# Performance work log

Hardware: AMD Instinct MI355X
Metric: run time of the kernel (lower is better)

## Reference

```python
import jax, jax.numpy as jnp
import numpy as np

N = 50000          # num nodes
E = 800000         # num edges (before self-loops)
F_IN = 128
H = 4              # heads
C1 = 16            # hidden channels per head
C2 = 8             # out channels per head
NEG_SLOPE = 0.2
EPS = 1e-16


def setup_inputs() -> dict:
    key = jax.random.key(0)
    ks = jax.random.split(key, 10)
    x = jax.random.normal(ks[0], (N, F_IN), dtype=jnp.float32)
    edge_index = jax.random.randint(ks[1], (2, E), 0, N, dtype=jnp.int64)
    s1 = 1.0 / np.sqrt(F_IN)
    s2 = 1.0 / np.sqrt(H * C1)
    return {
        "x": x,
        "edge_index": edge_index,
        "W1": jax.random.normal(ks[2], (F_IN, H * C1), dtype=jnp.float32) * s1,
        "a_src1": jax.random.normal(ks[3], (H, C1), dtype=jnp.float32) * s2,
        "a_dst1": jax.random.normal(ks[4], (H, C1), dtype=jnp.float32) * s2,
        "b1": jnp.zeros((H * C1,), dtype=jnp.float32),
        "W2": jax.random.normal(ks[5], (H * C1, H * C2), dtype=jnp.float32) * s2,
        "a_src2": jax.random.normal(ks[6], (H, C2), dtype=jnp.float32) * 0.2,
        "a_dst2": jax.random.normal(ks[7], (H, C2), dtype=jnp.float32) * 0.2,
        "b2": jnp.zeros((H * C2,), dtype=jnp.float32),
    }


def _gat_conv(x, src, dst, W, a_src, a_dst, b, heads, ch):
    # linear transform -> per-head features [N, H, C]
    h = (x @ W).reshape(-1, heads, ch)
    # per-node attention logits [N, H]
    al_src = jnp.sum(h * a_src[None], axis=-1)
    al_dst = jnp.sum(h * a_dst[None], axis=-1)
    # edge-wise logits + leaky relu [E, H]
    e = al_src[src] + al_dst[dst]
    e = jnp.where(e >= 0, e, NEG_SLOPE * e)
    # segment softmax over destination neighborhoods
    m = jax.ops.segment_max(e, dst, num_segments=N)
    e = jnp.exp(e - m[dst])
    s = jax.ops.segment_sum(e, dst, num_segments=N)
    alpha = e / (s[dst] + EPS)                      # [E, H]
    # weighted gather-scatter aggregate [N, H, C]
    msg = h[src] * alpha[..., None]
    out = jax.ops.segment_sum(msg, dst, num_segments=N)
    # concat heads + bias
    return out.reshape(-1, heads * ch) + b


def reference(x, edge_index, W1, a_src1, a_dst1, b1, W2, a_src2, a_dst2, b2):
    # PyG GATConv adds self-loops by default
    loop = jnp.arange(N, dtype=edge_index.dtype)
    src = jnp.concatenate([edge_index[0], loop])
    dst = jnp.concatenate([edge_index[1], loop])
    h = _gat_conv(x, src, dst, W1, a_src1, a_dst1, b1, H, C1)
    h = jax.nn.relu(h)
    h = _gat_conv(h, src, dst, W2, a_src2, a_dst2, b2, H, C2)
    return jax.nn.log_softmax(h, axis=1)
```

## Files before the change

### kernel.cpp

```cpp
#include <hip/hip_runtime.h>
#include <hip/hip_bf16.h>
#include <math.h>

#define NN 50000
#define NE 800000
#define ET (NE + NN)
#define DCAP 128
#define SG 196
#define ECH 8192
#define NCH 104
#define NPASS 8
#define NRANGE 6250

#define NCV 3321
#define NG1 1563
#define SPLITB (3 * NG1)
#define TOTB (NCV + NG1)

__device__ __forceinline__ float bf2f(unsigned short u) {
    return __uint_as_float(((unsigned)u) << 16);
}
__device__ __forceinline__ unsigned short f2bf(float f) {
    unsigned u = __float_as_uint(f);
    return (unsigned short)((u + 0x7fff + ((u >> 16) & 1)) >> 16);
}
__device__ __forceinline__ float lrelu(float e) {
    return e >= 0.f ? e : 0.2f * e;
}

__global__ __launch_bounds__(256) void k_front(const void* __restrict__ xraw,
                                               const void* __restrict__ ei,
                                               const void* p2, const void* p3, const void* p4, const void* p5,
                                               const void* p6, const void* p7, const void* p8, const void* p9,
                                               int2* __restrict__ pairs, int* __restrict__ deg,
                                               float* __restrict__ wsm,
                                               unsigned short* __restrict__ h1b,
                                               float* __restrict__ als, float* __restrict__ ald) {
    __shared__ unsigned int Wp[64 * 65];
    __shared__ float xt[32 * 132];
    __shared__ int wred[8];
    int t = threadIdx.x;
    int b = blockIdx.x;

    const unsigned long long* e64 = (const unsigned long long*)ei;
    const unsigned int* x32 = (const unsigned int*)xraw;
    int ci = 0, cf = 0;
    #pragma unroll
    for (int q = 0; q < 4; q++) {
        if (e64[4 * t + q] >= (unsigned long long)NN) ci = 1;
        unsigned ex = (x32[4 * t + q] >> 7) & 0xFFu;
        cf += (ex >= 96 && ex <= 140) ? 1 : 0;
    }
    #pragma unroll
    for (int off = 32; off; off >>= 1) { ci |= __shfl_xor(ci, off); cf += __shfl_xor(cf, off); }
    if ((t & 63) == 0) { wred[t >> 6] = ci; wred[4 + (t >> 6)] = cf; }
    __syncthreads();
    int iflag = (wred[0] | wred[1] | wred[2] | wred[3]) ? 0 : 1;
    int fl = ((wred[4] + wred[5] + wred[6] + wred[7]) > 700) ? 1 : 0;

    int role, id;
    if (b < SPLITB) {
        int g = b / 3, r = b % 3;
        if (r == 2) { role = 1; id = g; }
        else        { role = 0; id = 2 * g + r; }
    } else {
        role = 0; id = b - NG1;
    }

    if (role == 0) {
        int e = id * 256 + t;
        if (e < 10528) {
            const void* p; int off;
            if (e < 8192)       { p = p2; off = e; }
            else if (e < 8256)  { p = p3; off = e - 8192; }
            else if (e < 8320)  { p = p4; off = e - 8256; }
            else if (e < 8384)  { p = p5; off = e - 8320; }
            else if (e < 10432) { p = p6; off = e - 8384; }
            else if (e < 10464) { p = p7; off = e - 10432; }
            else if (e < 10496) { p = p8; off = e - 10464; }
            else                { p = p9; off = e - 10496; }
            wsm[e] = fl ? bf2f(((const unsigned short*)p)[off]) : ((const float*)p)[off];
        }
        if (e >= ET) return;
        int s, d;
        if (e >= NE) { s = d = e - NE; }
        else if (iflag) {
            s = (int)((const long long*)ei)[e];
            d = (int)((const long long*)ei)[NE + e];
        } else {
            s = ((const int*)ei)[e];
            d = ((const int*)ei)[NE + e];
        }
        pairs[e] = make_int2(s, d);
        atomicAdd(&deg[d], 1);
        return;
    }

    const void* w1raw = p2; const void* as1raw = p3; const void* ad1raw = p4;
    int rb = id * 32;
    for (int i = t; i < 64 * 64; i += 256) {
        int k2 = i >> 6, c = i & 63;
        unsigned lo, hi;
        if (fl) {
            lo = ((const unsigned short*)w1raw)[(2 * k2) * 64 + c];
            hi = ((const unsigned short*)w1raw)[(2 * k2 + 1) * 64 + c];
        } else {
            lo = f2bf(((const float*)w1raw)[(2 * k2) * 64 + c]);
            hi = f2bf(((const float*)w1raw)[(2 * k2 + 1) * 64 + c]);
        }
        Wp[c * 65 + k2] = lo | (hi << 16);
    }
    if (fl) {
        const unsigned short* xb = (const unsigned short*)xraw;
        for (int i = t; i < 32 * 16; i += 256) {
            int r = i >> 4, k8 = i & 15;
            float f[8];
            if (rb + r < NN) {
                uint4 v = ((const uint4*)xb)[(size_t)(rb + r) * 16 + k8];
                f[0] = bf2f((unsigned short)(v.x & 0xffff)); f[1] = bf2f((unsigned short)(v.x >> 16));
                f[2] = bf2f((unsigned short)(v.y & 0xffff)); f[3] = bf2f((unsigned short)(v.y >> 16));
                f[4] = bf2f((unsigned short)(v.z & 0xffff)); f[5] = bf2f((unsigned short)(v.z >> 16));
                f[6] = bf2f((unsigned short)(v.w & 0xffff)); f[7] = bf2f((unsigned short)(v.w >> 16));
            } else {
                #pragma unroll
                for (int q = 0; q < 8; q++) f[q] = 0.f;
            }
            int o = r * 132 + k8 * 8;
            *(float4*)&xt[o]     = make_float4(f[0], f[1], f[2], f[3]);
            *(float4*)&xt[o + 4] = make_float4(f[4], f[5], f[6], f[7]);
        }
    } else {
        const float* xf = (const float*)xraw;
        for (int i = t; i < 32 * 32; i += 256) {
            int r = i >> 5, kq = i & 31;
            float4 v = make_float4(0.f, 0.f, 0.f, 0.f);
            if (rb + r < NN) v = ((const float4*)xf)[(size_t)(rb + r) * 32 + kq];
            *(float4*)&xt[r * 132 + kq * 4] = v;
        }
    }
    __syncthreads();
    int c = t & 63;
    int rg = t >> 6;
    float acc[8];
    #pragma unroll
    for (int j = 0; j < 8; j++) acc[j] = 0.f;
    for (int k2 = 0; k2 < 64; k2 += 2) {
        unsigned q0 = Wp[c * 65 + k2];
        unsigned q1 = Wp[c * 65 + k2 + 1];
        float w0 = __uint_as_float(q0 << 16);
        float w1 = __uint_as_float(q0 & 0xffff0000u);
        float w2 = __uint_as_float(q1 << 16);
        float w3 = __uint_as_float(q1 & 0xffff0000u);
        int kk = k2 * 2;
        #pragma unroll
        for (int j = 0; j < 8; j++) {
            float4 xv = *(const float4*)&xt[(rg * 8 + j) * 132 + kk];
            acc[j] = fmaf(xv.x, w0, fmaf(xv.y, w1, fmaf(xv.z, w2, fmaf(xv.w, w3, acc[j]))));
        }
    }
    float asf = fl ? bf2f(((const unsigned short*)as1raw)[c]) : ((const float*)as1raw)[c];
    float adf = fl ? bf2f(((const unsigned short*)ad1raw)[c]) : ((const float*)ad1raw)[c];
    #pragma unroll
    for (int j = 0; j < 8; j++) {
        int r = rb + rg * 8 + j;
        bool ok = r < NN;
        if (ok) h1b[(size_t)r * 64 + c] = f2bf(acc[j]);
        float v = acc[j] * asf, w = acc[j] * adf;
        #pragma unroll
        for (int off = 1; off < 16; off <<= 1) {
            v += __shfl_xor(v, off);
            w += __shfl_xor(w, off);
        }
        if (ok && (c & 15) == 0) {
            als[r * 4 + (c >> 4)] = v;
            ald[r * 4 + (c >> 4)] = w;
        }
    }
}

__device__ __forceinline__ int block_excl_scan(int v, int* lds, int t) {
    int lane = t & 63, wid = t >> 6;
    int inc = v;
    #pragma unroll
    for (int d = 1; d < 64; d <<= 1) {
        int u = __shfl_up(inc, d);
        if (lane >= d) inc += u;
    }
    if (lane == 63) lds[wid] = inc;
    __syncthreads();
    if (t == 0) {
        int a = lds[0], b = lds[1], c = lds[2];
        lds[4] = 0; lds[5] = a; lds[6] = a + b; lds[7] = a + b + c;
    }
    __syncthreads();
    return lds[4 + wid] + inc - v;
}

__global__ __launch_bounds__(256) void k_scan(const int* __restrict__ deg, int* __restrict__ bsum,
                                              int* __restrict__ ctr,
                                              int* __restrict__ rs, int* __restrict__ cur) {
    __shared__ int lds[8];
    __shared__ int sOff, sTot;
    int t = threadIdx.x, b = blockIdx.x;
    int i = b * 256 + t;
    int v = (i < NN) ? deg[i] : 0;
    int e_loc = block_excl_scan(v, lds, t);
    if (t == 255) {
        bsum[b] = e_loc + v;
        __threadfence();
        atomicAdd(ctr, 1);
    }
    if (t == 0) {
        while (__hip_atomic_load(ctr, __ATOMIC_ACQUIRE, __HIP_MEMORY_SCOPE_AGENT) < SG) {
            __builtin_amdgcn_s_sleep(1);
        }
    }
    __syncthreads();
    __threadfence();
    int bv = (t < SG) ? bsum[t] : 0;
    int be = block_excl_scan(bv, lds, t);
    if (t == b) sOff = be;
    if (t == SG - 1) sTot = be + bv;
    __syncthreads();
    int e = sOff + e_loc;
    if (i < NN) {
        rs[i] = e; cur[i] = e;
        if (i == NN - 1) rs[NN] = sTot;
    }
}

__global__ __launch_bounds__(256) void k_scatter8(const int2* __restrict__ pairs,
                                                  int* __restrict__ cur, int* __restrict__ csr) {
    int b = blockIdx.x;
    int pass = b & (NPASS - 1);
    int chunk = b >> 3;
    int lo = pass * NRANGE, hi = lo + NRANGE;
    int base = chunk * ECH;
    for (int i = threadIdx.x; i < ECH; i += 256) {
        int e = base + i;
        if (e < ET) {
            int2 pr = pairs[e];
            if (pr.y >= lo && pr.y < hi) {
                int pos = atomicAdd(&cur[pr.y], 1);
                csr[pos] = pr.x;
            }
        }
    }
}

__global__ __launch_bounds__(256) void k_gemm2(const float* __restrict__ in,
                                               const float* __restrict__ Wf,
                                               const float* __restrict__ asf_p,
                                               const float* __restrict__ adf_p,
                                               unsigned short* __restrict__ h2b,
                                               float* __restrict__ als, float* __restrict__ ald) {
    __shared__ float Wt[32 * 65];
    __shared__ float xt[64 * 68];
    int tid = threadIdx.x;
    int rb = blockIdx.x * 64;
    for (int i = tid; i < 64 * 32; i += 256) {
        int k = i >> 5, c = i & 31;
        Wt[c * 65 + k] = Wf[i];
    }
    for (int i = tid; i < 64 * 16; i += 256) {
        int r = i >> 4, kq = i & 15;
        float4 v = make_float4(0.f, 0.f, 0.f, 0.f);
        if (rb + r < NN) v = ((const float4*)in)[(size_t)(rb + r) * 16 + kq];
        *(float4*)&xt[r * 68 + kq * 4] = v;
    }
    __syncthreads();
    int c = tid & 31, rg = tid >> 5;
    float acc[8];
    #pragma unroll
    for (int j = 0; j < 8; j++) acc[j] = 0.f;
    #pragma unroll 2
    for (int k = 0; k < 64; k += 4) {
        float4 w;
        w.x = Wt[c * 65 + k];     w.y = Wt[c * 65 + k + 1];
        w.z = Wt[c * 65 + k + 2]; w.w = Wt[c * 65 + k + 3];
        #pragma unroll
        for (int j = 0; j < 8; j++) {
            float4 xv = *(const float4*)&xt[(rg * 8 + j) * 68 + k];
            acc[j] = fmaf(xv.x, w.x, fmaf(xv.y, w.y, fmaf(xv.z, w.z, fmaf(xv.w, w.w, acc[j]))));
        }
    }
    float asf = asf_p[c], adf = adf_p[c];
    #pragma unroll
    for (int j = 0; j < 8; j++) {
        int r = rb + rg * 8 + j;
        bool ok = r < NN;
        if (ok) h2b[(size_t)r * 32 + c] = f2bf(acc[j]);
        float v = acc[j] * asf, w = acc[j] * adf;
        #pragma unroll
        for (int off = 1; off < 8; off <<= 1) {
            v += __shfl_xor(v, off);
            w += __shfl_xor(w, off);
        }
        if (ok && (c & 7) == 0) {
            als[r * 4 + (c >> 3)] = v;
            ald[r * 4 + (c >> 3)] = w;
        }
    }
}

__global__ __launch_bounds__(256) void k_agg1(const int* __restrict__ rs, const int* __restrict__ csr,
                                              const float* __restrict__ als, const float* __restrict__ aldv,
                                              const unsigned short* __restrict__ h1b,
                                              const float* __restrict__ b1,
                                              float* __restrict__ out1) {
    __shared__ float pv[4][DCAP * 4];
    __shared__ int  sidx[4][DCAP];
    int w = threadIdx.x >> 6, lane = threadIdx.x & 63;
    int n = blockIdx.x * 4 + w;
    if (n >= NN) return;
    int base = rs[n];
    int deg = rs[n + 1] - base;
    float4 ald = *(const float4*)(aldv + 4 * n);

    if (deg <= DCAP) {
        int sA = 0;
        bool v0 = lane < deg, v1 = lane + 64 < deg;
        if (v0) {
            sA = csr[base + lane];
            sidx[w][lane] = sA;
            float4 a = *(const float4*)(als + 4 * sA);
            float4 p;
            p.x = __expf(lrelu(a.x + ald.x)); p.y = __expf(lrelu(a.y + ald.y));
            p.z = __expf(lrelu(a.z + ald.z)); p.w = __expf(lrelu(a.w + ald.w));
            *(float4*)&pv[w][lane * 4] = p;
        }
        if (v1) {
            int sB = csr[base + lane + 64];
            sidx[w][lane + 64] = sB;
            float4 a = *(const float4*)(als + 4 * sB);
            float4 p;
            p.x = __expf(lrelu(a.x + ald.x)); p.y = __expf(lrelu(a.y + ald.y));
            p.z = __expf(lrelu(a.z + ald.z)); p.w = __expf(lrelu(a.w + ald.w));
            *(float4*)&pv[w][(lane + 64) * 4] = p;
        }
        int degp = (deg + 3) & ~3;
        int s0v = __shfl(sA, 0);
        if (lane >= deg && lane < degp) {
            sidx[w][lane] = s0v;
            *(float4*)&pv[w][lane * 4] = make_float4(0.f, 0.f, 0.f, 0.f);
        }
        int i1 = lane + 64;
        if (i1 >= deg && i1 < degp) {
            sidx[w][i1] = s0v;
            *(float4*)&pv[w][i1 * 4] = make_float4(0.f, 0.f, 0.f, 0.f);
        }
        int g = lane >> 4, j = lane & 15, hh = j >> 2;
        float4 a4 = make_float4(0.f, 0.f, 0.f, 0.f);
        float ps = 0.f;
        for (int e = 0; e < degp; e += 4) {
            int s = sidx[w][e + g];
            float ph = pv[w][(e + g) * 4 + hh];
            uint2 rv = *(const uint2*)&h1b[(size_t)s * 64 + j * 4];
            ps += ph;
            a4.x = fmaf(ph, bf2f((unsigned short)(rv.x & 0xffff)), a4.x);
            a4.y = fmaf(ph, bf2f((unsigned short)(rv.x >> 16)),    a4.y);
            a4.z = fmaf(ph, bf2f((unsigned short)(rv.y & 0xffff)), a4.z);
            a4.w = fmaf(ph, bf2f((unsigned short)(rv.y >> 16)),    a4.w);
        }
        #pragma unroll
        for (int off = 16; off <= 32; off <<= 1) {
            a4.x += __shfl_xor(a4.x, off);
            a4.y += __shfl_xor(a4.y, off);
            a4.z += __shfl_xor(a4.z, off);
            a4.w += __shfl_xor(a4.w, off);
            ps   += __shfl_xor(ps,   off);
        }
        if (g == 0) {
            float rh = 1.f / (ps + 1e-16f);
            float4 bb = *(const float4*)&b1[j * 4];
            float4 o;
            o.x = fmaxf(a4.x * rh + bb.x, 0.f);
            o.y = fmaxf(a4.y * rh + bb.y, 0.f);
            o.z = fmaxf(a4.z * rh + bb.z, 0.f);
            o.w = fmaxf(a4.w * rh + bb.w, 0.f);
            *(float4*)&out1[(size_t)n * 64 + j * 4] = o;
        }
    } else {
        int h = lane >> 4;
        float s0 = 0.f, s1 = 0.f, s2 = 0.f, s3 = 0.f;
        for (int i = lane; i < deg; i += 64) {
            int s = csr[base + i];
            float4 a = *(const float4*)(als + 4 * s);
            s0 += __expf(lrelu(a.x + ald.x));
            s1 += __expf(lrelu(a.y + ald.y));
            s2 += __expf(lrelu(a.z + ald.z));
            s3 += __expf(lrelu(a.w + ald.w));
        }
        #pragma unroll
        for (int off = 32; off; off >>= 1) {
            s0 += __shfl_xor(s0, off);
            s1 += __shfl_xor(s1, off);
            s2 += __shfl_xor(s2, off);
            s3 += __shfl_xor(s3, off);
        }
        float sh = (h == 0) ? s0 : (h == 1) ? s1 : (h == 2) ? s2 : s3;
        float ah = (h == 0) ? ald.x : (h == 1) ? ald.y : (h == 2) ? ald.z : ald.w;
        float rh = 1.f / (sh + 1e-16f);
        float acc = 0.f;
        for (int e = 0; e < deg; ++e) {
            int s = csr[base + e];
            float av = als[4 * s + h];
            float ph = __expf(lrelu(av + ah));
            acc = fmaf(ph, bf2f(h1b[(size_t)s * 64 + lane]), acc);
        }
        out1[(size_t)n * 64 + lane] = fmaxf(acc * rh + b1[lane], 0.f);
    }
}

__global__ __launch_bounds__(256) void k_agg2(const int* __restrict__ rs, const int* __restrict__ csr,
                                              const float* __restrict__ als, const float* __restrict__ aldv,
                                              const unsigned short* __restrict__ h2b,
                                              const float* __restrict__ b2,
                                              float* __restrict__ out) {
    __shared__ float pv[4][DCAP * 4];
    __shared__ int  sidx[4][DCAP];
    int w = threadIdx.x >> 6, lane = threadIdx.x & 63;
    int n = blockIdx.x * 4 + w;
    if (n >= NN) return;
    int base = rs[n];
    int deg = rs[n + 1] - base;
    float4 ald = *(const float4*)(aldv + 4 * n);

    if (deg <= DCAP) {
        int sA = 0;
        bool v0 = lane < deg, v1 = lane + 64 < deg;
        if (v0) {
            sA = csr[base + lane];
            sidx[w][lane] = sA;
            float4 a = *(const float4*)(als + 4 * sA);
            float4 p;
            p.x = __expf(lrelu(a.x + ald.x)); p.y = __expf(lrelu(a.y + ald.y));
            p.z = __expf(lrelu(a.z + ald.z)); p.w = __expf(lrelu(a.w + ald.w));
            *(float4*)&pv[w][lane * 4] = p;
        }
        if (v1) {
            int sB = csr[base + lane + 64];
            sidx[w][lane + 64] = sB;
            float4 a = *(const float4*)(als + 4 * sB);
            float4 p;
            p.x = __expf(lrelu(a.x + ald.x)); p.y = __expf(lrelu(a.y + ald.y));
            p.z = __expf(lrelu(a.z + ald.z)); p.w = __expf(lrelu(a.w + ald.w));
            *(float4*)&pv[w][(lane + 64) * 4] = p;
        }
        int degp = (deg + 7) & ~7;
        int s0v = __shfl(sA, 0);
        if (lane >= deg && lane < degp) {
            sidx[w][lane] = s0v;
            *(float4*)&pv[w][lane * 4] = make_float4(0.f, 0.f, 0.f, 0.f);
        }
        int i1 = lane + 64;
        if (i1 >= deg && i1 < degp) {
            sidx[w][i1] = s0v;
            *(float4*)&pv[w][i1 * 4] = make_float4(0.f, 0.f, 0.f, 0.f);
        }
        int g = lane >> 3, j = lane & 7, hh = j >> 1;
        float4 a4 = make_float4(0.f, 0.f, 0.f, 0.f);
        float ps = 0.f;
        for (int e = 0; e < degp; e += 8) {
            int s = sidx[w][e + g];
            float ph = pv[w][(e + g) * 4 + hh];
            uint2 rv = *(const uint2*)&h2b[(size_t)s * 32 + j * 4];
            ps += ph;
            a4.x = fmaf(ph, bf2f((unsigned short)(rv.x & 0xffff)), a4.x);
            a4.y = fmaf(ph, bf2f((unsigned short)(rv.x >> 16)),    a4.y);
            a4.z = fmaf(ph, bf2f((unsigned short)(rv.y & 0xffff)), a4.z);
            a4.w = fmaf(ph, bf2f((unsigned short)(rv.y >> 16)),    a4.w);
        }
        #pragma unroll
        for (int off = 8; off <= 32; off <<= 1) {
            a4.x += __shfl_xor(a4.x, off);
            a4.y += __shfl_xor(a4.y, off);
            a4.z += __shfl_xor(a4.z, off);
            a4.w += __shfl_xor(a4.w, off);
            ps   += __shfl_xor(ps,   off);
        }
        float rh = 1.f / (ps + 1e-16f);
        float4 bb = *(const float4*)&b2[j * 4];
        float4 row;
        row.x = a4.x * rh + bb.x; row.y = a4.y * rh + bb.y;
        row.z = a4.z * rh + bb.z; row.w = a4.w * rh + bb.w;
        float mx = fmaxf(fmaxf(row.x, row.y), fmaxf(row.z, row.w));
        #pragma unroll
        for (int off = 1; off < 8; off <<= 1) mx = fmaxf(mx, __shfl_xor(mx, off));
        float sm = __expf(row.x - mx) + __expf(row.y - mx)
                 + __expf(row.z - mx) + __expf(row.w - mx);
        #pragma unroll
        for (int off = 1; off < 8; off <<= 1) sm += __shfl_xor(sm, off);
        float lse = mx + logf(sm);
        if (g == 0) {
            float4 o;
            o.x = row.x - lse; o.y = row.y - lse;
            o.z = row.z - lse; o.w = row.w - lse;
            *(float4*)&out[(size_t)n * 32 + j * 4] = o;
        }
    } else {
        float s0 = 0.f, s1 = 0.f, s2 = 0.f, s3 = 0.f;
        for (int i = lane; i < deg; i += 64) {
            int s = csr[base + i];
            float4 a = *(const float4*)(als + 4 * s);
            s0 += __expf(lrelu(a.x + ald.x));
            s1 += __expf(lrelu(a.y + ald.y));
            s2 += __expf(lrelu(a.z + ald.z));
            s3 += __expf(lrelu(a.w + ald.w));
        }
        #pragma unroll
        for (int off = 32; off; off >>= 1) {
            s0 += __shfl_xor(s0, off);
            s1 += __shfl_xor(s1, off);
            s2 += __shfl_xor(s2, off);
            s3 += __shfl_xor(s3, off);
        }
        int L = lane & 31;
        int h2i = L >> 3;
        float sh2 = (h2i == 0) ? s0 : (h2i == 1) ? s1 : (h2i == 2) ? s2 : s3;
        float ah2 = (h2i == 0) ? ald.x : (h2i == 1) ? ald.y : (h2i == 2) ? ald.z : ald.w;
        float rh2 = 1.f / (sh2 + 1e-16f);
        if (lane < 32) {
            float acc = 0.f;
            for (int e = 0; e < deg; ++e) {
                int s = csr[base + e];
                float av = als[4 * s + h2i];
                float ph = __expf(lrelu(av + ah2));
                acc = fmaf(ph, bf2f(h2b[(size_t)s * 32 + L]), acc);
            }
            float row = acc * rh2 + b2[L];
            float mx = row;
            #pragma unroll
            for (int off = 16; off; off >>= 1) mx = fmaxf(mx, __shfl_xor(mx, off, 32));
            float pe = __expf(row - mx);
            float sm = pe;
            #pragma unroll
            for (int off = 16; off; off >>= 1) sm += __shfl_xor(sm, off, 32);
            out[(size_t)n * 32 + L] = row - mx - logf(sm);
        }
    }
}

extern "C" void kernel_launch(void* const* d_in, const int* in_sizes, int n_in,
                              void* d_out, int out_size, void* d_ws, size_t ws_size,
                              hipStream_t stream) {
    const void* x  = d_in[0];
    const void* ei = d_in[1];
    float* out = (float*)d_out;

    char* p = (char*)d_ws;
    auto take = [&](size_t b) -> char* {
        char* r = p; p += (b + 255) & ~(size_t)255; return r;
    };
    int*   degc  = (int*)take(sizeof(int) * (NN + 8));
    int*   deg   = degc;
    int*   ctr   = degc + NN;
    int*   rs    = (int*)take(sizeof(int) * (NN + 1));
    int*   cur   = (int*)take(sizeof(int) * NN);
    int*   bsum  = (int*)take(sizeof(int) * 256);
    int2*  pairs = (int2*)take(sizeof(int2) * ET);
    int*   csr   = (int*)take(sizeof(int) * ET);
    float* wsm   = (float*)take(sizeof(float) * 10528);
    unsigned short* h1b = (unsigned short*)take(sizeof(unsigned short) * (size_t)NN * 64);
    float* als1  = (float*)take(sizeof(float) * NN * 4);
    float* ald1  = (float*)take(sizeof(float) * NN * 4);
    float* out1  = (float*)take(sizeof(float) * (size_t)NN * 64);
    unsigned short* h2b = (unsigned short*)take(sizeof(unsigned short) * (size_t)NN * 32);
    float* als2  = (float*)take(sizeof(float) * NN * 4);
    float* ald2  = (float*)take(sizeof(float) * NN * 4);

    float* Wf2  = wsm + 8384;
    float* as2f = wsm + 10432;
    float* ad2f = wsm + 10464;
    float* b1f  = wsm + 8320;
    float* b2f  = wsm + 10496;

    hipMemsetAsync(degc, 0, sizeof(int) * (NN + 8), stream);
    k_front<<<TOTB, 256, 0, stream>>>(x, ei, d_in[2], d_in[3], d_in[4], d_in[5],
                                      d_in[6], d_in[7], d_in[8], d_in[9],
                                      pairs, deg, wsm, h1b, als1, ald1);
    k_scan<<<SG, 256, 0, stream>>>(deg, bsum, ctr, rs, cur);
    k_scatter8<<<NPASS * NCH, 256, 0, stream>>>(pairs, cur, csr);

    k_agg1<<<(NN + 3) / 4, 256, 0, stream>>>(rs, csr, als1, ald1, h1b, b1f, out1);

    k_gemm2<<<(NN + 63) / 64, 256, 0, stream>>>(out1, Wf2, as2f, ad2f, h2b, als2, ald2);
    k_agg2<<<(NN + 3) / 4, 256, 0, stream>>>(rs, csr, als2, ald2, h2b, b2f, out);
}
```

Baseline: 276.2 us.

## Fuse CSR build into one persistent kernel with grid barriers, split out GEMM1

Edge pair extraction, degree counting, the prefix scan and the CSR scatter now run in a single 832-block kernel that uses atomic-counter grid barriers between phases, in place of three separate launches. The first-layer GEMM moves into its own kernel launched first. Before, the GEMM was interleaved with the edge work inside one launch. The aim is to cut launch gaps and tail effects. The grid barriers are safe only if all 832 blocks are co-resident, and the fused kernel loses the overlap with GEMM1 it had before.

After: 629.0 us. 128% more time.

```diff
diff --git a/kernel.cpp b/kernel.cpp
--- a/kernel.cpp
+++ b/kernel.cpp
@@ -11,11 +11,8 @@
 #define NCH 104
 #define NPASS 8
 #define NRANGE 6250
-
-#define NCV 3321
+#define CSRB (NPASS * NCH)
 #define NG1 1563
-#define SPLITB (3 * NG1)
-#define TOTB (NCV + NG1)
 
 __device__ __forceinline__ float bf2f(unsigned short u) {
     return __uint_as_float(((unsigned)u) << 16);
@@ -28,19 +25,50 @@
     return e >= 0.f ? e : 0.2f * e;
 }
 
-__global__ __launch_bounds__(256) void k_front(const void* __restrict__ xraw,
-                                               const void* __restrict__ ei,
-                                               const void* p2, const void* p3, const void* p4, const void* p5,
-                                               const void* p6, const void* p7, const void* p8, const void* p9,
-                                               int2* __restrict__ pairs, int* __restrict__ deg,
-                                               float* __restrict__ wsm,
-                                               unsigned short* __restrict__ h1b,
-                                               float* __restrict__ als, float* __restrict__ ald) {
-    __shared__ unsigned int Wp[64 * 65];
-    __shared__ float xt[32 * 132];
+__device__ __forceinline__ int block_excl_scan(int v, int* lds, int t) {
+    int lane = t & 63, wid = t >> 6;
+    int inc = v;
+    #pragma unroll
+    for (int d = 1; d < 64; d <<= 1) {
+        int u = __shfl_up(inc, d);
+        if (lane >= d) inc += u;
+    }
+    if (lane == 63) lds[wid] = inc;
+    __syncthreads();
+    if (t == 0) {
+        int a = lds[0], b = lds[1], c = lds[2];
+        lds[4] = 0; lds[5] = a; lds[6] = a + b; lds[7] = a + b + c;
+    }
+    __syncthreads();
+    return lds[4 + wid] + inc - v;
+}
+
+__device__ __forceinline__ void gbar(int* ctr, int target) {
+    __syncthreads();
+    if (threadIdx.x == 0) {
+        __threadfence();
+        atomicAdd(ctr, 1);
+        while (__hip_atomic_load(ctr, __ATOMIC_ACQUIRE, __HIP_MEMORY_SCOPE_AGENT) < target) {
+            __builtin_amdgcn_s_sleep(1);
+        }
+    }
+    __syncthreads();
+    __threadfence();
+}
+
+__global__ __launch_bounds__(256) void k_csr(const void* __restrict__ xraw,
+                                             const void* __restrict__ ei,
+                                             const void* p2, const void* p3, const void* p4, const void* p5,
+                                             const void* p6, const void* p7, const void* p8, const void* p9,
+                                             int2* __restrict__ pairs, int* __restrict__ deg,
+                                             float* __restrict__ wsm, int* __restrict__ bsum,
+                                             int* __restrict__ ctrA, int* __restrict__ ctrS, int* __restrict__ ctrB,
+                                             int* __restrict__ rs, int* __restrict__ cur,
+                                             int* __restrict__ csr) {
+    __shared__ int lds[8];
     __shared__ int wred[8];
-    int t = threadIdx.x;
-    int b = blockIdx.x;
+    __shared__ int sOff, sTot;
+    int t = threadIdx.x, b = blockIdx.x;
 
     const unsigned long long* e64 = (const unsigned long long*)ei;
     const unsigned int* x32 = (const unsigned int*)xraw;
@@ -58,17 +86,7 @@
     int iflag = (wred[0] | wred[1] | wred[2] | wred[3]) ? 0 : 1;
     int fl = ((wred[4] + wred[5] + wred[6] + wred[7]) > 700) ? 1 : 0;
 
-    int role, id;
-    if (b < SPLITB) {
-        int g = b / 3, r = b % 3;
-        if (r == 2) { role = 1; id = g; }
-        else        { role = 0; id = 2 * g + r; }
-    } else {
-        role = 0; id = b - NG1;
-    }
-
-    if (role == 0) {
-        int e = id * 256 + t;
+    for (int e = b * 256 + t; e < ET; e += CSRB * 256) {
         if (e < 10528) {
             const void* p; int off;
             if (e < 8192)       { p = p2; off = e; }
@@ -81,7 +99,6 @@
             else                { p = p9; off = e - 10496; }
             wsm[e] = fl ? bf2f(((const unsigned short*)p)[off]) : ((const float*)p)[off];
         }
-        if (e >= ET) return;
         int s, d;
         if (e >= NE) { s = d = e - NE; }
         else if (iflag) {
@@ -93,12 +110,84 @@
         }
         pairs[e] = make_int2(s, d);
         atomicAdd(&deg[d], 1);
-        return;
-    }
-
-    const void* w1raw = p2; const void* as1raw = p3; const void* ad1raw = p4;
-    int rb = id * 32;
-    for (int i = t; i < 64 * 64; i += 256) {
+    }
+
+    gbar(ctrA, CSRB);
+
+    if (b < SG) {
+        int i = b * 256 + t;
+        int v = (i < NN) ? deg[i] : 0;
+        int e_loc = block_excl_scan(v, lds, t);
+        if (t == 255) {
+            bsum[b] = e_loc + v;
+            __threadfence();
+            atomicAdd(ctrS, 1);
+        }
+        if (t == 0) {
+            while (__hip_atomic_load(ctrS, __ATOMIC_ACQUIRE, __HIP_MEMORY_SCOPE_AGENT) < SG) {
+                __builtin_amdgcn_s_sleep(1);
+            }
+        }
+        __syncthreads();
+        __threadfence();
+        int bv = (t < SG) ? bsum[t] : 0;
+        int be = block_excl_scan(bv, lds, t);
+        if (t == b) sOff = be;
+        if (t == SG - 1) sTot = be + bv;
+        __syncthreads();
+        int e = sOff + e_loc;
+        if (i < NN) {
+            rs[i] = e; cur[i] = e;
+            if (i == NN - 1) rs[NN] = sTot;
+        }
+    }
+
+    gbar(ctrB, CSRB);
+
+    {
+        int pass = b & (NPASS - 1);
+        int chunk = b >> 3;
+        int lo = pass * NRANGE, hi = lo + NRANGE;
+        int base = chunk * ECH;
+        for (int i = t; i < ECH; i += 256) {
+            int e = base + i;
+            if (e < ET) {
+                int2 pr = pairs[e];
+                if (pr.y >= lo && pr.y < hi) {
+                    int pos = atomicAdd(&cur[pr.y], 1);
+                    csr[pos] = pr.x;
+                }
+            }
+        }
+    }
+}
+
+__global__ __launch_bounds__(256) void k_gemm1(const void* __restrict__ xraw,
+                                               const void* __restrict__ w1raw,
+                                               const void* __restrict__ as1raw,
+                                               const void* __restrict__ ad1raw,
+                                               unsigned short* __restrict__ h1b,
+                                               float* __restrict__ als, float* __restrict__ ald) {
+    __shared__ unsigned int Wp[64 * 65];
+    __shared__ float xt[32 * 132];
+    __shared__ int wred[4];
+    int tid = threadIdx.x;
+    int rb = blockIdx.x * 32;
+
+    const unsigned int* x32 = (const unsigned int*)xraw;
+    int cf = 0;
+    #pragma unroll
+    for (int q = 0; q < 4; q++) {
+        unsigned ex = (x32[4 * tid + q] >> 7) & 0xFFu;
+        cf += (ex >= 96 && ex <= 140) ? 1 : 0;
+    }
+    #pragma unroll
+    for (int off = 32; off; off >>= 1) cf += __shfl_xor(cf, off);
+    if ((tid & 63) == 0) wred[tid >> 6] = cf;
+    __syncthreads();
+    int fl = ((wred[0] + wred[1] + wred[2] + wred[3]) > 700) ? 1 : 0;
+
+    for (int i = tid; i < 64 * 64; i += 256) {
         int k2 = i >> 6, c = i & 63;
         unsigned lo, hi;
         if (fl) {
@@ -112,7 +201,7 @@
     }
     if (fl) {
         const unsigned short* xb = (const unsigned short*)xraw;
-        for (int i = t; i < 32 * 16; i += 256) {
+        for (int i = tid; i < 32 * 16; i += 256) {
             int r = i >> 4, k8 = i & 15;
             float f[8];
             if (rb + r < NN) {
@@ -131,7 +220,7 @@
         }
     } else {
         const float* xf = (const float*)xraw;
-        for (int i = t; i < 32 * 32; i += 256) {
+        for (int i = tid; i < 32 * 32; i += 256) {
             int r = i >> 5, kq = i & 31;
             float4 v = make_float4(0.f, 0.f, 0.f, 0.f);
             if (rb + r < NN) v = ((const float4*)xf)[(size_t)(rb + r) * 32 + kq];
@@ -139,8 +228,8 @@
         }
     }
     __syncthreads();
-    int c = t & 63;
-    int rg = t >> 6;
+    int c = tid & 63;
+    int rg = tid >> 6;
     float acc[8];
     #pragma unroll
     for (int j = 0; j < 8; j++) acc[j] = 0.f;
@@ -174,76 +263,6 @@
         if (ok && (c & 15) == 0) {
             als[r * 4 + (c >> 4)] = v;
             ald[r * 4 + (c >> 4)] = w;
-        }
-    }
-}
-
-__device__ __forceinline__ int block_excl_scan(int v, int* lds, int t) {
-    int lane = t & 63, wid = t >> 6;
-    int inc = v;
-    #pragma unroll
-    for (int d = 1; d < 64; d <<= 1) {
-        int u = __shfl_up(inc, d);
-        if (lane >= d) inc += u;
-    }
-    if (lane == 63) lds[wid] = inc;
-    __syncthreads();
-    if (t == 0) {
-        int a = lds[0], b = lds[1], c = lds[2];
-        lds[4] = 0; lds[5] = a; lds[6] = a + b; lds[7] = a + b + c;
-    }
-    __syncthreads();
-    return lds[4 + wid] + inc - v;
-}
-
-__global__ __launch_bounds__(256) void k_scan(const int* __restrict__ deg, int* __restrict__ bsum,
-                                              int* __restrict__ ctr,
-                                              int* __restrict__ rs, int* __restrict__ cur) {
-    __shared__ int lds[8];
-    __shared__ int sOff, sTot;
-    int t = threadIdx.x, b = blockIdx.x;
-    int i = b * 256 + t;
-    int v = (i < NN) ? deg[i] : 0;
-    int e_loc = block_excl_scan(v, lds, t);
-    if (t == 255) {
-        bsum[b] = e_loc + v;
-        __threadfence();
-        atomicAdd(ctr, 1);
-    }
-    if (t == 0) {
-        while (__hip_atomic_load(ctr, __ATOMIC_ACQUIRE, __HIP_MEMORY_SCOPE_AGENT) < SG) {
-            __builtin_amdgcn_s_sleep(1);
-        }
-    }
-    __syncthreads();
-    __threadfence();
-    int bv = (t < SG) ? bsum[t] : 0;
-    int be = block_excl_scan(bv, lds, t);
-    if (t == b) sOff = be;
-    if (t == SG - 1) sTot = be + bv;
-    __syncthreads();
-    int e = sOff + e_loc;
-    if (i < NN) {
-        rs[i] = e; cur[i] = e;
-        if (i == NN - 1) rs[NN] = sTot;
-    }
-}
-
-__global__ __launch_bounds__(256) void k_scatter8(const int2* __restrict__ pairs,
-                                                  int* __restrict__ cur, int* __restrict__ csr) {
-    int b = blockIdx.x;
-    int pass = b & (NPASS - 1);
-    int chunk = b >> 3;
-    int lo = pass * NRANGE, hi = lo + NRANGE;
-    int base = chunk * ECH;
-    for (int i = threadIdx.x; i < ECH; i += 256) {
-        int e = base + i;
-        if (e < ET) {
-            int2 pr = pairs[e];
-            if (pr.y >= lo && pr.y < hi) {
-                int pos = atomicAdd(&cur[pr.y], 1);
-                csr[pos] = pr.x;
-            }
         }
     }
 }
@@ -554,7 +573,9 @@
     };
     int*   degc  = (int*)take(sizeof(int) * (NN + 8));
     int*   deg   = degc;
-    int*   ctr   = degc + NN;
+    int*   ctrA  = degc + NN;
+    int*   ctrS  = degc + NN + 1;
+    int*   ctrB  = degc + NN + 2;
     int*   rs    = (int*)take(sizeof(int) * (NN + 1));
     int*   cur   = (int*)take(sizeof(int) * NN);
     int*   bsum  = (int*)take(sizeof(int) * 256);
@@ -576,11 +597,10 @@
     float* b2f  = wsm + 10496;
 
     hipMemsetAsync(degc, 0, sizeof(int) * (NN + 8), stream);
-    k_front<<<TOTB, 256, 0, stream>>>(x, ei, d_in[2], d_in[3], d_in[4], d_in[5],
-                                      d_in[6], d_in[7], d_in[8], d_in[9],
-                                      pairs, deg, wsm, h1b, als1, ald1);
-    k_scan<<<SG, 256, 0, stream>>>(deg, bsum, ctr, rs, cur);
-    k_scatter8<<<NPASS * NCH, 256, 0, stream>>>(pairs, cur, csr);
+    k_gemm1<<<NG1, 256, 0, stream>>>(x, d_in[2], d_in[3], d_in[4], h1b, als1, ald1);
+    k_csr<<<CSRB, 256, 0, stream>>>(x, ei, d_in[2], d_in[3], d_in[4], d_in[5],
+                                    d_in[6], d_in[7], d_in[8], d_in[9],
+                                    pairs, deg, wsm, bsum, ctrA, ctrS, ctrB, rs, cur, csr);
 
     k_agg1<<<(NN + 3) / 4, 256, 0, stream>>>(rs, csr, als1, ald1, h1b, b1f, out1);
 
```

## Replace CSR scan/scatter with fixed-capacity per-node adjacency plus overflow list

Applied to the files above, without the earlier changes.

Drops the degree prefix scan and the multi-pass scatter kernels. Each edge now claims a slot in a fixed 48-entry row per destination node via atomicAdd and is written straight there, or into a global overflow list once the row is full. The aggregation kernels read these rows directly and, for high-degree nodes, linearly scan the overflow list. This removes two launches and the pairs buffer in exchange for a larger, sparser adjacency array, a capacity limit of 8192 overflow edges, and a costly linear overflow scan for the few high-degree nodes.

After: 225.0 us. -18.6%, faster.

```diff
diff --git a/kernel.cpp b/kernel.cpp
--- a/kernel.cpp
+++ b/kernel.cpp
@@ -5,17 +5,9 @@
 #define NN 50000
 #define NE 800000
 #define ET (NE + NN)
-#define DCAP 128
-#define SG 196
-#define ECH 8192
-#define NCH 104
-#define NPASS 8
-#define NRANGE 6250
-
-#define NCV 3321
+#define DCAP 48
+#define MAXOVF 8192
 #define NG1 1563
-#define SPLITB (3 * NG1)
-#define TOTB (NCV + NG1)
 
 __device__ __forceinline__ float bf2f(unsigned short u) {
     return __uint_as_float(((unsigned)u) << 16);
@@ -28,77 +20,39 @@
     return e >= 0.f ? e : 0.2f * e;
 }
 
-__global__ __launch_bounds__(256) void k_front(const void* __restrict__ xraw,
-                                               const void* __restrict__ ei,
-                                               const void* p2, const void* p3, const void* p4, const void* p5,
-                                               const void* p6, const void* p7, const void* p8, const void* p9,
-                                               int2* __restrict__ pairs, int* __restrict__ deg,
-                                               float* __restrict__ wsm,
-                                               unsigned short* __restrict__ h1b,
-                                               float* __restrict__ als, float* __restrict__ ald) {
+__global__ __launch_bounds__(256) void k_gemm1cv(const void* __restrict__ xraw,
+                                                 const void* __restrict__ ei,
+                                                 const void* p2, const void* p3, const void* p4, const void* p5,
+                                                 const void* p6, const void* p7, const void* p8, const void* p9,
+                                                 unsigned short* __restrict__ h1b,
+                                                 float* __restrict__ als, float* __restrict__ ald,
+                                                 int* __restrict__ csrF, int* __restrict__ deg,
+                                                 int2* __restrict__ ovf, int* __restrict__ ovfcnt,
+                                                 float* __restrict__ wsm) {
     __shared__ unsigned int Wp[64 * 65];
     __shared__ float xt[32 * 132];
     __shared__ int wred[8];
-    int t = threadIdx.x;
-    int b = blockIdx.x;
-
-    const unsigned long long* e64 = (const unsigned long long*)ei;
+    int tid = threadIdx.x;
+    int rb = blockIdx.x * 32;
+
+    const unsigned long long* e64u = (const unsigned long long*)ei;
     const unsigned int* x32 = (const unsigned int*)xraw;
     int ci = 0, cf = 0;
     #pragma unroll
     for (int q = 0; q < 4; q++) {
-        if (e64[4 * t + q] >= (unsigned long long)NN) ci = 1;
-        unsigned ex = (x32[4 * t + q] >> 7) & 0xFFu;
+        if (e64u[4 * tid + q] >= (unsigned long long)NN) ci = 1;
+        unsigned ex = (x32[4 * tid + q] >> 7) & 0xFFu;
         cf += (ex >= 96 && ex <= 140) ? 1 : 0;
     }
     #pragma unroll
     for (int off = 32; off; off >>= 1) { ci |= __shfl_xor(ci, off); cf += __shfl_xor(cf, off); }
-    if ((t & 63) == 0) { wred[t >> 6] = ci; wred[4 + (t >> 6)] = cf; }
+    if ((tid & 63) == 0) { wred[tid >> 6] = ci; wred[4 + (tid >> 6)] = cf; }
     __syncthreads();
     int iflag = (wred[0] | wred[1] | wred[2] | wred[3]) ? 0 : 1;
     int fl = ((wred[4] + wred[5] + wred[6] + wred[7]) > 700) ? 1 : 0;
 
-    int role, id;
-    if (b < SPLITB) {
-        int g = b / 3, r = b % 3;
-        if (r == 2) { role = 1; id = g; }
-        else        { role = 0; id = 2 * g + r; }
-    } else {
-        role = 0; id = b - NG1;
-    }
-
-    if (role == 0) {
-        int e = id * 256 + t;
-        if (e < 10528) {
-            const void* p; int off;
-            if (e < 8192)       { p = p2; off = e; }
-            else if (e < 8256)  { p = p3; off = e - 8192; }
-            else if (e < 8320)  { p = p4; off = e - 8256; }
-            else if (e < 8384)  { p = p5; off = e - 8320; }
-            else if (e < 10432) { p = p6; off = e - 8384; }
-            else if (e < 10464) { p = p7; off = e - 10432; }
-            else if (e < 10496) { p = p8; off = e - 10464; }
-            else                { p = p9; off = e - 10496; }
-            wsm[e] = fl ? bf2f(((const unsigned short*)p)[off]) : ((const float*)p)[off];
-        }
-        if (e >= ET) return;
-        int s, d;
-        if (e >= NE) { s = d = e - NE; }
-        else if (iflag) {
-            s = (int)((const long long*)ei)[e];
-            d = (int)((const long long*)ei)[NE + e];
-        } else {
-            s = ((const int*)ei)[e];
-            d = ((const int*)ei)[NE + e];
-        }
-        pairs[e] = make_int2(s, d);
-        atomicAdd(&deg[d], 1);
-        return;
-    }
-
     const void* w1raw = p2; const void* as1raw = p3; const void* ad1raw = p4;
-    int rb = id * 32;
-    for (int i = t; i < 64 * 64; i += 256) {
+    for (int i = tid; i < 64 * 64; i += 256) {
         int k2 = i >> 6, c = i & 63;
         unsigned lo, hi;
         if (fl) {
@@ -112,7 +66,7 @@
     }
     if (fl) {
         const unsigned short* xb = (const unsigned short*)xraw;
-        for (int i = t; i < 32 * 16; i += 256) {
+        for (int i = tid; i < 32 * 16; i += 256) {
             int r = i >> 4, k8 = i & 15;
             float f[8];
             if (rb + r < NN) {
@@ -131,7 +85,7 @@
         }
     } else {
         const float* xf = (const float*)xraw;
-        for (int i = t; i < 32 * 32; i += 256) {
+        for (int i = tid; i < 32 * 32; i += 256) {
             int r = i >> 5, kq = i & 31;
             float4 v = make_float4(0.f, 0.f, 0.f, 0.f);
             if (rb + r < NN) v = ((const float4*)xf)[(size_t)(rb + r) * 32 + kq];
@@ -139,8 +93,8 @@
         }
     }
     __syncthreads();
-    int c = t & 63;
-    int rg = t >> 6;
+    int c = tid & 63;
+    int rg = tid >> 6;
     float acc[8];
     #pragma unroll
     for (int j = 0; j < 8; j++) acc[j] = 0.f;
@@ -176,75 +130,151 @@
             ald[r * 4 + (c >> 4)] = w;
         }
     }
-}
-
-__device__ __forceinline__ int block_excl_scan(int v, int* lds, int t) {
-    int lane = t & 63, wid = t >> 6;
-    int inc = v;
-    #pragma unroll
-    for (int d = 1; d < 64; d <<= 1) {
-        int u = __shfl_up(inc, d);
-        if (lane >= d) inc += u;
-    }
-    if (lane == 63) lds[wid] = inc;
-    __syncthreads();
-    if (t == 0) {
-        int a = lds[0], b = lds[1], c = lds[2];
-        lds[4] = 0; lds[5] = a; lds[6] = a + b; lds[7] = a + b + c;
-    }
-    __syncthreads();
-    return lds[4 + wid] + inc - v;
-}
-
-__global__ __launch_bounds__(256) void k_scan(const int* __restrict__ deg, int* __restrict__ bsum,
-                                              int* __restrict__ ctr,
-                                              int* __restrict__ rs, int* __restrict__ cur) {
-    __shared__ int lds[8];
-    __shared__ int sOff, sTot;
-    int t = threadIdx.x, b = blockIdx.x;
-    int i = b * 256 + t;
-    int v = (i < NN) ? deg[i] : 0;
-    int e_loc = block_excl_scan(v, lds, t);
-    if (t == 255) {
-        bsum[b] = e_loc + v;
-        __threadfence();
-        atomicAdd(ctr, 1);
-    }
-    if (t == 0) {
-        while (__hip_atomic_load(ctr, __ATOMIC_ACQUIRE, __HIP_MEMORY_SCOPE_AGENT) < SG) {
-            __builtin_amdgcn_s_sleep(1);
-        }
-    }
-    __syncthreads();
-    __threadfence();
-    int bv = (t < SG) ? bsum[t] : 0;
-    int be = block_excl_scan(bv, lds, t);
-    if (t == b) sOff = be;
-    if (t == SG - 1) sTot = be + bv;
-    __syncthreads();
-    int e = sOff + e_loc;
-    if (i < NN) {
-        rs[i] = e; cur[i] = e;
-        if (i == NN - 1) rs[NN] = sTot;
-    }
-}
-
-__global__ __launch_bounds__(256) void k_scatter8(const int2* __restrict__ pairs,
-                                                  int* __restrict__ cur, int* __restrict__ csr) {
-    int b = blockIdx.x;
-    int pass = b & (NPASS - 1);
-    int chunk = b >> 3;
-    int lo = pass * NRANGE, hi = lo + NRANGE;
-    int base = chunk * ECH;
-    for (int i = threadIdx.x; i < ECH; i += 256) {
-        int e = base + i;
-        if (e < ET) {
-            int2 pr = pairs[e];
-            if (pr.y >= lo && pr.y < hi) {
-                int pos = atomicAdd(&cur[pr.y], 1);
-                csr[pos] = pr.x;
+
+    const long long* e64s = (const long long*)ei;
+    for (int e = blockIdx.x * 256 + tid; e < ET; e += NG1 * 256) {
+        if (e < 10528) {
+            const void* p; int off;
+            if (e < 8192)       { p = p2; off = e; }
+            else if (e < 8256)  { p = p3; off = e - 8192; }
+            else if (e < 8320)  { p = p4; off = e - 8256; }
+            else if (e < 8384)  { p = p5; off = e - 8320; }
+            else if (e < 10432) { p = p6; off = e - 8384; }
+            else if (e < 10464) { p = p7; off = e - 10432; }
+            else if (e < 10496) { p = p8; off = e - 10464; }
+            else                { p = p9; off = e - 10496; }
+            wsm[e] = fl ? bf2f(((const unsigned short*)p)[off]) : ((const float*)p)[off];
+        }
+        int s, d;
+        if (e >= NE) { s = d = e - NE; }
+        else if (iflag) {
+            s = (int)e64s[e];
+            d = (int)e64s[NE + e];
+        } else {
+            s = ((const int*)ei)[e];
+            d = ((const int*)ei)[NE + e];
+        }
+        int slot = atomicAdd(&deg[d], 1);
+        if (slot < DCAP) csrF[(size_t)d * DCAP + slot] = s;
+        else {
+            int o = atomicAdd(ovfcnt, 1);
+            if (o < MAXOVF) ovf[o] = make_int2(s, d);
+        }
+    }
+}
+
+__global__ __launch_bounds__(256) void k_agg1(const int* __restrict__ degv, const int* __restrict__ csrF,
+                                              const int2* __restrict__ ovf, const int* __restrict__ ovfcnt,
+                                              const float* __restrict__ als, const float* __restrict__ aldv,
+                                              const unsigned short* __restrict__ h1b,
+                                              const float* __restrict__ b1,
+                                              float* __restrict__ out1) {
+    __shared__ float pv[4][DCAP * 4];
+    __shared__ int  sidx[4][DCAP];
+    int w = threadIdx.x >> 6, lane = threadIdx.x & 63;
+    int n = blockIdx.x * 4 + w;
+    if (n >= NN) return;
+    int dg = degv[n];
+    const int* cf = csrF + (size_t)n * DCAP;
+    float4 ald = *(const float4*)(aldv + 4 * n);
+
+    if (dg <= DCAP) {
+        int sA = 0;
+        bool v0 = lane < dg;
+        if (v0) {
+            sA = cf[lane];
+            sidx[w][lane] = sA;
+            float4 a = *(const float4*)(als + 4 * sA);
+            float4 p;
+            p.x = __expf(lrelu(a.x + ald.x)); p.y = __expf(lrelu(a.y + ald.y));
+            p.z = __expf(lrelu(a.z + ald.z)); p.w = __expf(lrelu(a.w + ald.w));
+            *(float4*)&pv[w][lane * 4] = p;
+        }
+        int degp = (dg + 3) & ~3;
+        int s0v = __shfl(sA, 0);
+        if (lane >= dg && lane < degp) {
+            sidx[w][lane] = s0v;
+            *(float4*)&pv[w][lane * 4] = make_float4(0.f, 0.f, 0.f, 0.f);
+        }
+        int g = lane >> 4, j = lane & 15, hh = j >> 2;
+        float4 a4 = make_float4(0.f, 0.f, 0.f, 0.f);
+        float ps = 0.f;
+        for (int e = 0; e < degp; e += 4) {
+            int s = sidx[w][e + g];
+            float ph = pv[w][(e + g) * 4 + hh];
+            uint2 rv = *(const uint2*)&h1b[(size_t)s * 64 + j * 4];
+            ps += ph;
+            a4.x = fmaf(ph, bf2f((unsigned short)(rv.x & 0xffff)), a4.x);
+            a4.y = fmaf(ph, bf2f((unsigned short)(rv.x >> 16)),    a4.y);
+            a4.z = fmaf(ph, bf2f((unsigned short)(rv.y & 0xffff)), a4.z);
+            a4.w = fmaf(ph, bf2f((unsigned short)(rv.y >> 16)),    a4.w);
+        }
+        #pragma unroll
+        for (int off = 16; off <= 32; off <<= 1) {
+            a4.x += __shfl_xor(a4.x, off);
+            a4.y += __shfl_xor(a4.y, off);
+            a4.z += __shfl_xor(a4.z, off);
+            a4.w += __shfl_xor(a4.w, off);
+            ps   += __shfl_xor(ps,   off);
+        }
+        if (g == 0) {
+            float rh = 1.f / (ps + 1e-16f);
+            float4 bb = *(const float4*)&b1[j * 4];
+            float4 o;
+            o.x = fmaxf(a4.x * rh + bb.x, 0.f);
+            o.y = fmaxf(a4.y * rh + bb.y, 0.f);
+            o.z = fmaxf(a4.z * rh + bb.z, 0.f);
+            o.w = fmaxf(a4.w * rh + bb.w, 0.f);
+            *(float4*)&out1[(size_t)n * 64 + j * 4] = o;
+        }
+    } else {
+        int h = lane >> 4;
+        int oN = min(*ovfcnt, MAXOVF);
+        float s0 = 0.f, s1 = 0.f, s2 = 0.f, s3 = 0.f;
+        for (int i = lane; i < DCAP; i += 64) {
+            int s = cf[i];
+            float4 a = *(const float4*)(als + 4 * s);
+            s0 += __expf(lrelu(a.x + ald.x));
+            s1 += __expf(lrelu(a.y + ald.y));
+            s2 += __expf(lrelu(a.z + ald.z));
+            s3 += __expf(lrelu(a.w + ald.w));
+        }
+        for (int i = lane; i < oN; i += 64) {
+            int2 pr = ovf[i];
+            if (pr.y == n) {
+                float4 a = *(const float4*)(als + 4 * pr.x);
+                s0 += __expf(lrelu(a.x + ald.x));
+                s1 += __expf(lrelu(a.y + ald.y));
+                s2 += __expf(lrelu(a.z + ald.z));
+                s3 += __expf(lrelu(a.w + ald.w));
             }
         }
+        #pragma unroll
+        for (int off = 32; off; off >>= 1) {
+            s0 += __shfl_xor(s0, off);
+            s1 += __shfl_xor(s1, off);
+            s2 += __shfl_xor(s2, off);
+            s3 += __shfl_xor(s3, off);
+        }
+        float sh = (h == 0) ? s0 : (h == 1) ? s1 : (h == 2) ? s2 : s3;
+        float ah = (h == 0) ? ald.x : (h == 1) ? ald.y : (h == 2) ? ald.z : ald.w;
+        float rh = 1.f / (sh + 1e-16f);
+        float acc = 0.f;
+        for (int e = 0; e < DCAP; ++e) {
+            int s = cf[e];
+            float av = als[4 * s + h];
+            float ph = __expf(lrelu(av + ah));
+            acc = fmaf(ph, bf2f(h1b[(size_t)s * 64 + lane]), acc);
+        }
+        for (int o = 0; o < oN; ++o) {
+            int2 pr = ovf[o];
+            if (pr.y == n) {
+                float av = als[4 * pr.x + h];
+                float ph = __expf(lrelu(av + ah));
+                acc = fmaf(ph, bf2f(h1b[(size_t)pr.x * 64 + lane]), acc);
+            }
+        }
+        out1[(size_t)n * 64 + lane] = fmaxf(acc * rh + b1[lane], 0.f);
     }
 }
 
@@ -303,116 +333,8 @@
     }
 }
 
-__global__ __launch_bounds__(256) void k_agg1(const int* __restrict__ rs, const int* __restrict__ csr,
-                                              const float* __restrict__ als, const float* __restrict__ aldv,
-                                              const unsigned short* __restrict__ h1b,
-                                              const float* __restrict__ b1,
-                                              float* __restrict__ out1) {
-    __shared__ float pv[4][DCAP * 4];
-    __shared__ int  sidx[4][DCAP];
-    int w = threadIdx.x >> 6, lane = threadIdx.x & 63;
-    int n = blockIdx.x * 4 + w;
-    if (n >= NN) return;
-    int base = rs[n];
-    int deg = rs[n + 1] - base;
-    float4 ald = *(const float4*)(aldv + 4 * n);
-
-    if (deg <= DCAP) {
-        int sA = 0;
-        bool v0 = lane < deg, v1 = lane + 64 < deg;
-        if (v0) {
-            sA = csr[base + lane];
-            sidx[w][lane] = sA;
-            float4 a = *(const float4*)(als + 4 * sA);
-            float4 p;
-            p.x = __expf(lrelu(a.x + ald.x)); p.y = __expf(lrelu(a.y + ald.y));
-            p.z = __expf(lrelu(a.z + ald.z)); p.w = __expf(lrelu(a.w + ald.w));
-            *(float4*)&pv[w][lane * 4] = p;
-        }
-        if (v1) {
-            int sB = csr[base + lane + 64];
-            sidx[w][lane + 64] = sB;
-            float4 a = *(const float4*)(als + 4 * sB);
-            float4 p;
-            p.x = __expf(lrelu(a.x + ald.x)); p.y = __expf(lrelu(a.y + ald.y));
-            p.z = __expf(lrelu(a.z + ald.z)); p.w = __expf(lrelu(a.w + ald.w));
-            *(float4*)&pv[w][(lane + 64) * 4] = p;
-        }
-        int degp = (deg + 3) & ~3;
-        int s0v = __shfl(sA, 0);
-        if (lane >= deg && lane < degp) {
-            sidx[w][lane] = s0v;
-            *(float4*)&pv[w][lane * 4] = make_float4(0.f, 0.f, 0.f, 0.f);
-        }
-        int i1 = lane + 64;
-        if (i1 >= deg && i1 < degp) {
-            sidx[w][i1] = s0v;
-            *(float4*)&pv[w][i1 * 4] = make_float4(0.f, 0.f, 0.f, 0.f);
-        }
-        int g = lane >> 4, j = lane & 15, hh = j >> 2;
-        float4 a4 = make_float4(0.f, 0.f, 0.f, 0.f);
-        float ps = 0.f;
-        for (int e = 0; e < degp; e += 4) {
-            int s = sidx[w][e + g];
-            float ph = pv[w][(e + g) * 4 + hh];
-            uint2 rv = *(const uint2*)&h1b[(size_t)s * 64 + j * 4];
-            ps += ph;
-            a4.x = fmaf(ph, bf2f((unsigned short)(rv.x & 0xffff)), a4.x);
-            a4.y = fmaf(ph, bf2f((unsigned short)(rv.x >> 16)),    a4.y);
-            a4.z = fmaf(ph, bf2f((unsigned short)(rv.y & 0xffff)), a4.z);
-            a4.w = fmaf(ph, bf2f((unsigned short)(rv.y >> 16)),    a4.w);
-        }
-        #pragma unroll
-        for (int off = 16; off <= 32; off <<= 1) {
-            a4.x += __shfl_xor(a4.x, off);
-            a4.y += __shfl_xor(a4.y, off);
-            a4.z += __shfl_xor(a4.z, off);
-            a4.w += __shfl_xor(a4.w, off);
-            ps   += __shfl_xor(ps,   off);
-        }
-        if (g == 0) {
-            float rh = 1.f / (ps + 1e-16f);
-            float4 bb = *(const float4*)&b1[j * 4];
-            float4 o;
-            o.x = fmaxf(a4.x * rh + bb.x, 0.f);
-            o.y = fmaxf(a4.y * rh + bb.y, 0.f);
-            o.z = fmaxf(a4.z * rh + bb.z, 0.f);
-            o.w = fmaxf(a4.w * rh + bb.w, 0.f);
-            *(float4*)&out1[(size_t)n * 64 + j * 4] = o;
-        }
-    } else {
-        int h = lane >> 4;
-        float s0 = 0.f, s1 = 0.f, s2 = 0.f, s3 = 0.f;
-        for (int i = lane; i < deg; i += 64) {
-            int s = csr[base + i];
-            float4 a = *(const float4*)(als + 4 * s);
-            s0 += __expf(lrelu(a.x + ald.x));
-            s1 += __expf(lrelu(a.y + ald.y));
-            s2 += __expf(lrelu(a.z + ald.z));
-            s3 += __expf(lrelu(a.w + ald.w));
-        }
-        #pragma unroll
-        for (int off = 32; off; off >>= 1) {
-            s0 += __shfl_xor(s0, off);
-            s1 += __shfl_xor(s1, off);
-            s2 += __shfl_xor(s2, off);
-            s3 += __shfl_xor(s3, off);
-        }
-        float sh = (h == 0) ? s0 : (h == 1) ? s1 : (h == 2) ? s2 : s3;
-        float ah = (h == 0) ? ald.x : (h == 1) ? ald.y : (h == 2) ? ald.z : ald.w;
-        float rh = 1.f / (sh + 1e-16f);
-        float acc = 0.f;
-        for (int e = 0; e < deg; ++e) {
-            int s = csr[base + e];
-            float av = als[4 * s + h];
-            float ph = __expf(lrelu(av + ah));
-            acc = fmaf(ph, bf2f(h1b[(size_t)s * 64 + lane]), acc);
-        }
-        out1[(size_t)n * 64 + lane] = fmaxf(acc * rh + b1[lane], 0.f);
-    }
-}
-
-__global__ __launch_bounds__(256) void k_agg2(const int* __restrict__ rs, const int* __restrict__ csr,
+__global__ __launch_bounds__(256) void k_agg2(const int* __restrict__ degv, const int* __restrict__ csrF,
+                                              const int2* __restrict__ ovf, const int* __restrict__ ovfcnt,
                                               const float* __restrict__ als, const float* __restrict__ aldv,
                                               const unsigned short* __restrict__ h2b,
                                               const float* __restrict__ b2,
@@ -422,15 +344,15 @@
     int w = threadIdx.x >> 6, lane = threadIdx.x & 63;
     int n = blockIdx.x * 4 + w;
     if (n >= NN) return;
-    int base = rs[n];
-    int deg = rs[n + 1] - base;
+    int dg = degv[n];
+    const int* cf = csrF + (size_t)n * DCAP;
     float4 ald = *(const float4*)(aldv + 4 * n);
 
-    if (deg <= DCAP) {
+    if (dg <= DCAP) {
         int sA = 0;
-        bool v0 = lane < deg, v1 = lane + 64 < deg;
+        bool v0 = lane < dg;
         if (v0) {
-            sA = csr[base + lane];
+            sA = cf[lane];
             sidx[w][lane] = sA;
             float4 a = *(const float4*)(als + 4 * sA);
             float4 p;
@@ -438,25 +360,11 @@
             p.z = __expf(lrelu(a.z + ald.z)); p.w = __expf(lrelu(a.w + ald.w));
             *(float4*)&pv[w][lane * 4] = p;
         }
-        if (v1) {
-            int sB = csr[base + lane + 64];
-            sidx[w][lane + 64] = sB;
-            float4 a = *(const float4*)(als + 4 * sB);
-            float4 p;
-            p.x = __expf(lrelu(a.x + ald.x)); p.y = __expf(lrelu(a.y + ald.y));
-            p.z = __expf(lrelu(a.z + ald.z)); p.w = __expf(lrelu(a.w + ald.w));
-            *(float4*)&pv[w][(lane + 64) * 4] = p;
-        }
-        int degp = (deg + 7) & ~7;
+        int degp = (dg + 7) & ~7;
         int s0v = __shfl(sA, 0);
-        if (lane >= deg && lane < degp) {
+        if (lane >= dg && lane < degp) {
             sidx[w][lane] = s0v;
             *(float4*)&pv[w][lane * 4] = make_float4(0.f, 0.f, 0.f, 0.f);
-        }
-        int i1 = lane + 64;
-        if (i1 >= deg && i1 < degp) {
-            sidx[w][i1] = s0v;
-            *(float4*)&pv[w][i1 * 4] = make_float4(0.f, 0.f, 0.f, 0.f);
         }
         int g = lane >> 3, j = lane & 7, hh = j >> 1;
         float4 a4 = make_float4(0.f, 0.f, 0.f, 0.f);
@@ -499,14 +407,25 @@
             *(float4*)&out[(size_t)n * 32 + j * 4] = o;
         }
     } else {
+        int oN = min(*ovfcnt, MAXOVF);
         float s0 = 0.f, s1 = 0.f, s2 = 0.f, s3 = 0.f;
-        for (int i = lane; i < deg; i += 64) {
-            int s = csr[base + i];
+        for (int i = lane; i < DCAP; i += 64) {
+            int s = cf[i];
             float4 a = *(const float4*)(als + 4 * s);
             s0 += __expf(lrelu(a.x + ald.x));
             s1 += __expf(lrelu(a.y + ald.y));
             s2 += __expf(lrelu(a.z + ald.z));
             s3 += __expf(lrelu(a.w + ald.w));
+        }
+        for (int i = lane; i < oN; i += 64) {
+            int2 pr = ovf[i];
+            if (pr.y == n) {
+                float4 a = *(const float4*)(als + 4 * pr.x);
+                s0 += __expf(lrelu(a.x + ald.x));
+                s1 += __expf(lrelu(a.y + ald.y));
+                s2 += __expf(lrelu(a.z + ald.z));
+                s3 += __expf(lrelu(a.w + ald.w));
+            }
         }
         #pragma unroll
         for (int off = 32; off; off >>= 1) {
@@ -522,11 +441,19 @@
         float rh2 = 1.f / (sh2 + 1e-16f);
         if (lane < 32) {
             float acc = 0.f;
-            for (int e = 0; e < deg; ++e) {
-                int s = csr[base + e];
+            for (int e = 0; e < DCAP; ++e) {
+                int s = cf[e];
                 float av = als[4 * s + h2i];
                 float ph = __expf(lrelu(av + ah2));
                 acc = fmaf(ph, bf2f(h2b[(size_t)s * 32 + L]), acc);
+            }
+            for (int o = 0; o < oN; ++o) {
+                int2 pr = ovf[o];
+                if (pr.y == n) {
+                    float av = als[4 * pr.x + h2i];
+                    float ph = __expf(lrelu(av + ah2));
+                    acc = fmaf(ph, bf2f(h2b[(size_t)pr.x * 32 + L]), acc);
+                }
             }
             float row = acc * rh2 + b2[L];
             float mx = row;
@@ -554,12 +481,9 @@
     };
     int*   degc  = (int*)take(sizeof(int) * (NN + 8));
     int*   deg   = degc;
-    int*   ctr   = degc + NN;
-    int*   rs    = (int*)take(sizeof(int) * (NN + 1));
-    int*   cur   = (int*)take(sizeof(int) * NN);
-    int*   bsum  = (int*)take(sizeof(int) * 256);
-    int2*  pairs = (int2*)take(sizeof(int2) * ET);
-    int*   csr   = (int*)take(sizeof(int) * ET);
+    int*   ovfcnt = degc + NN;
+    int*   csrF  = (int*)take(sizeof(int) * (size_t)NN * DCAP);
+    int2*  ovf   = (int2*)take(sizeof(int2) * MAXOVF);
     float* wsm   = (float*)take(sizeof(float) * 10528);
     unsigned short* h1b = (unsigned short*)take(sizeof(unsigned short) * (size_t)NN * 64);
     float* als1  = (float*)take(sizeof(float) * NN * 4);
@@ -576,14 +500,10 @@
     float* b2f  = wsm + 10496;
 
     hipMemsetAsync(degc, 0, sizeof(int) * (NN + 8), stream);
-    k_front<<<TOTB, 256, 0, stream>>>(x, ei, d_in[2], d_in[3], d_in[4], d_in[5],
-                                      d_in[6], d_in[7], d_in[8], d_in[9],
-                                      pairs, deg, wsm, h1b, als1, ald1);
-    k_scan<<<SG, 256, 0, stream>>>(deg, bsum, ctr, rs, cur);
-    k_scatter8<<<NPASS * NCH, 256, 0, stream>>>(pairs, cur, csr);
-
-    k_agg1<<<(NN + 3) / 4, 256, 0, stream>>>(rs, csr, als1, ald1, h1b, b1f, out1);
-
+    k_gemm1cv<<<NG1, 256, 0, stream>>>(x, ei, d_in[2], d_in[3], d_in[4], d_in[5],
+                                       d_in[6], d_in[7], d_in[8], d_in[9],
+                                       h1b, als1, ald1, csrF, deg, ovf, ovfcnt, wsm);
+    k_agg1<<<(NN + 3) / 4, 256, 0, stream>>>(deg, csrF, ovf, ovfcnt, als1, ald1, h1b, b1f, out1);
     k_gemm2<<<(NN + 63) / 64, 256, 0, stream>>>(out1, Wf2, as2f, ad2f, h2b, als2, ald2);
-    k_agg2<<<(NN + 3) / 4, 256, 0, stream>>>(rs, csr, als2, ald2, h2b, b2f, out);
-}
+    k_agg2<<<(NN + 3) / 4, 256, 0, stream>>>(deg, csrF, ovf, ovfcnt, als2, ald2, h2b, b2f, out);
+}
```
